# Performance work log

Measured on AMD Instinct MI355X. Metric: run time of the kernel, lower is better.

Reference implementation:

```python
import jax, jax.numpy as jnp
import numpy as np

N_NODES = 100000
N_EDGES = 3200000
IN_DIM = 64
HID = 64


def setup_inputs() -> dict:
    key = jax.random.key(0)
    ks = jax.random.split(key, 12)
    x = jax.random.normal(ks[0], (N_NODES, IN_DIM), dtype=jnp.float32)
    edge_index = jax.random.randint(ks[1], (2, N_EDGES), 0, N_NODES, dtype=jnp.int64)
    tau = jax.random.uniform(ks[2], (N_NODES, 1), dtype=jnp.float32)
    d1 = IN_DIM + 1  # augmented feature dim
    s1 = 1.0 / np.sqrt(d1)
    s2 = 1.0 / np.sqrt(HID)
    # SAGEConv: out = lin_l(mean_aggr) + lin_r(x); bias lives in lin_l. Weights stored [in, out].
    W1l = jax.random.uniform(ks[3], (d1, HID), jnp.float32, -s1, s1)
    b1l = jax.random.uniform(ks[4], (HID,), jnp.float32, -s1, s1)
    W1r = jax.random.uniform(ks[5], (d1, HID), jnp.float32, -s1, s1)
    W2l = jax.random.uniform(ks[6], (HID, HID), jnp.float32, -s2, s2)
    b2l = jax.random.uniform(ks[7], (HID,), jnp.float32, -s2, s2)
    W2r = jax.random.uniform(ks[8], (HID, HID), jnp.float32, -s2, s2)
    Wfc = jax.random.uniform(ks[9], (HID, 1), jnp.float32, -s2, s2)
    bfc = jax.random.uniform(ks[10], (1,), jnp.float32, -s2, s2)
    return {"x": x, "edge_index": edge_index, "tau": tau,
            "W1l": W1l, "b1l": b1l, "W1r": W1r,
            "W2l": W2l, "b2l": b2l, "W2r": W2r,
            "Wfc": Wfc, "bfc": bfc}


def _sage_conv(x, src, dst, Wl, bl, Wr, n_nodes):
    # mean aggregation of source-node features onto target nodes
    summed = jax.ops.segment_sum(x[src], dst, num_segments=n_nodes)  # [N, d]
    deg = jax.ops.segment_sum(jnp.ones(src.shape[0], x.dtype), dst, num_segments=n_nodes)
    mean = summed / jnp.maximum(deg, 1.0)[:, None]
    return mean @ Wl + bl + x @ Wr


def reference(x, edge_index, tau, W1l, b1l, W1r, W2l, b2l, W2r, Wfc, bfc):
    src, dst = edge_index[0], edge_index[1]
    n = x.shape[0]
    h = jnp.concatenate([x, tau], axis=1)  # augment_features: append tau column
    h = jax.nn.relu(_sage_conv(h, src, dst, W1l, b1l, W1r, n))
    h = jax.nn.relu(_sage_conv(h, src, dst, W2l, b2l, W2r, n))
    return h @ Wfc + bfc  # [N, 1]
```

## Files before the change

kernel.cpp:

```cpp
#include <hip/hip_runtime.h>
#include <hip/hip_bf16.h>
#include <hip/hip_fp16.h>


#define WAVES_PER_BLOCK 16
#define LAYER_BLOCK (WAVES_PER_BLOCK * 64)
#define LAYER_GRID 512

#define BSH 7
#define NBKT 782
#define NBLK 256

typedef _Float16 half8 __attribute__((ext_vector_type(8)));
typedef float floatx4 __attribute__((ext_vector_type(4)));


__global__ __launch_bounds__(256) void k_hist(const int* __restrict__ dst,
                                              int* __restrict__ histT, int E) {
    __shared__ int h[NBKT];
    for (int i = threadIdx.x; i < NBKT; i += 256) h[i] = 0;
    __syncthreads();
    int per = (E + NBLK - 1) / NBLK;
    int lo = blockIdx.x * per;
    int hi = lo + per; if (hi > E) hi = E;
    for (int e = lo + threadIdx.x; e < hi; e += 256)
        atomicAdd(&h[dst[e] >> BSH], 1);
    __syncthreads();
    for (int k = threadIdx.x; k < NBKT; k += 256)
        histT[k * NBLK + blockIdx.x] = h[k];
}

__global__ __launch_bounds__(NBLK) void k_scanblk(int* __restrict__ histT,
                                                  int* __restrict__ btot) {
    __shared__ int s[NBLK];
    int k = blockIdx.x, t = threadIdx.x;
    int v = histT[k * NBLK + t];
    s[t] = v;
    __syncthreads();
    for (int off = 1; off < NBLK; off <<= 1) {
        int u = (t >= off) ? s[t - off] : 0;
        __syncthreads();
        s[t] += u;
        __syncthreads();
    }
    histT[k * NBLK + t] = s[t] - v;
    if (t == NBLK - 1) btot[k] = s[t];
}

__global__ __launch_bounds__(1024) void k_scanbkt(const int* __restrict__ btot,
                                                  int* __restrict__ bstart) {
    __shared__ int s[1024];
    int t = threadIdx.x;
    int v = (t < NBKT) ? btot[t] : 0;
    s[t] = v;
    __syncthreads();
    for (int off = 1; off < 1024; off <<= 1) {
        int u = (t >= off) ? s[t - off] : 0;
        __syncthreads();
        s[t] += u;
        __syncthreads();
    }
    if (t < NBKT) bstart[t] = s[t] - v;
    if (t == NBKT - 1) bstart[NBKT] = s[t];
}

__global__ __launch_bounds__(256) void k_scatter(const int* __restrict__ src,
                                                 const int* __restrict__ dst,
                                                 const int* __restrict__ histT,
                                                 const int* __restrict__ bstart,
                                                 int* __restrict__ binned, int E) {
    __shared__ int cur[NBKT];
    int b = blockIdx.x;
    for (int k = threadIdx.x; k < NBKT; k += 256)
        cur[k] = bstart[k] + histT[k * NBLK + b];
    __syncthreads();
    int per = (E + NBLK - 1) / NBLK;
    int lo = b * per;
    int hi = lo + per; if (hi > E) hi = E;
    for (int e = lo + threadIdx.x; e < hi; e += 256) {
        int d = dst[e], s = src[e];
        int pos = atomicAdd(&cur[d >> BSH], 1);
        binned[pos] = (s << BSH) | (d & ((1 << BSH) - 1));
    }
}

__global__ __launch_bounds__(256) void k_bucket(const int* __restrict__ binned,
                                                const int* __restrict__ bstart,
                                                int* __restrict__ rowptr,
                                                int* __restrict__ deg,
                                                int* __restrict__ colidx, int N) {
    __shared__ int cnt[128], sc[128], cur[128];
    int k = blockIdx.x, t = threadIdx.x;
    int lo = bstart[k], hi = bstart[k + 1];
    if (t < 128) cnt[t] = 0;
    __syncthreads();
    for (int e = lo + t; e < hi; e += 256)
        atomicAdd(&cnt[binned[e] & 127], 1);
    __syncthreads();
    if (t < 128) sc[t] = cnt[t];
    __syncthreads();
    for (int off = 1; off < 128; off <<= 1) {
        int u = 0;
        if (t < 128 && t >= off) u = sc[t - off];
        __syncthreads();
        if (t < 128) sc[t] += u;
        __syncthreads();
    }
    if (t < 128) {
        int abs0 = lo + (sc[t] - cnt[t]);
        cur[t] = abs0;
        int gnode = (k << BSH) + t;
        if (gnode < N) { rowptr[gnode] = abs0; deg[gnode] = cnt[t]; }
    }
    __syncthreads();
    for (int e = lo + t; e < hi; e += 256) {
        int p = binned[e];
        int pos = atomicAdd(&cur[p & 127], 1);
        colidx[pos] = p >> BSH;
    }
}

__global__ __launch_bounds__(256) void k_prep(const float* __restrict__ x,
                                              __half* __restrict__ xh, int n2) {
    int i = blockIdx.x * 256 + threadIdx.x;
    if (i < n2) {
        float2 v = ((const float2*)x)[i];
        ((__half2*)xh)[i] = __floats2half2_rn(v.x, v.y);
    }
}

__global__ __launch_bounds__(256) void k_prepw(
    const float* __restrict__ W1l, const float* __restrict__ W1r,
    const float* __restrict__ W2l, const float* __restrict__ W2r,
    __half* __restrict__ wbuf1, __half* __restrict__ wbuf2) {
    int idx = blockIdx.x * 256 + threadIdx.x;
    if (idx < 1280) {
        int lane = idx & 63;
        int nt = (idx >> 6) & 3;
        int kstep = idx >> 8;
        int col = nt * 16 + (lane & 15);
        int kbase = kstep * 32 + (lane >> 4) * 8;
#pragma unroll
        for (int j = 0; j < 8; ++j) {
            int k = kbase + j;
            float v;
            if (k < 64)       v = W1l[k * 64 + col];
            else if (k < 128) v = W1r[(k - 64) * 64 + col];
            else if (k == 128) v = W1l[64 * 64 + col];
            else if (k == 129) v = W1r[64 * 64 + col];
            else v = 0.f;
            wbuf1[(size_t)idx * 8 + j] = __float2half(v);
        }
    } else if (idx < 1280 + 1024) {
        int i2 = idx - 1280;
        int lane = i2 & 63;
        int nt = (i2 >> 6) & 3;
        int kstep = i2 >> 8;
        int col = nt * 16 + (lane & 15);
        int kbase = kstep * 32 + (lane >> 4) * 8;
#pragma unroll
        for (int j = 0; j < 8; ++j) {
            int k = kbase + j;
            float v = (k < 64) ? W2l[k * 64 + col] : W2r[(k - 64) * 64 + col];
            wbuf2[(size_t)i2 * 8 + j] = __float2half(v);
        }
    }
}


__device__ __forceinline__ int pair_idx(int sidx, int j2, int half) {
    return __builtin_amdgcn_ds_bpermute(((j2 + half) << 2), sidx);
}

__global__ __launch_bounds__(LAYER_BLOCK) void k_aggr1(
    const __half* __restrict__ xh, const float* __restrict__ tau,
    const int* __restrict__ rowptr, const int* __restrict__ deg,
    const int* __restrict__ colidx,
    __half* __restrict__ zm1, __half* __restrict__ mt1, int N) {
    int lane = threadIdx.x & 63;
    int half = lane >> 5;
    int c2 = (lane & 31) << 1;
    int wave = blockIdx.x * WAVES_PER_BLOCK + (threadIdx.x >> 6);
    int nwaves = gridDim.x * WAVES_PER_BLOCK;

    for (int node = wave; node < N; node += nwaves) {
        int start = rowptr[node];
        int d = deg[node];
        float2 A0 = {0.f, 0.f}, A1 = {0.f, 0.f}, A2 = {0.f, 0.f}, A3 = {0.f, 0.f};
        float sumtau = 0.f;
        for (int base = 0; base < d; base += 64) {
            int n = d - base;
            if (n > 64) n = 64;
            int sidx = 0;
            if (lane < n) {
                sidx = colidx[start + base + lane];
                sumtau += tau[sidx];
            }
            int npair = n >> 1;
            int j = 0;
            for (; j + 4 <= npair; j += 4) {
                int i0 = pair_idx(sidx, (j + 0) << 1, half);
                int i1 = pair_idx(sidx, (j + 1) << 1, half);
                int i2 = pair_idx(sidx, (j + 2) << 1, half);
                int i3 = pair_idx(sidx, (j + 3) << 1, half);
                float2 v0 = __half22float2(*(const __half2*)(xh + ((size_t)(unsigned)i0 << 6) + c2));
                float2 v1 = __half22float2(*(const __half2*)(xh + ((size_t)(unsigned)i1 << 6) + c2));
                float2 v2 = __half22float2(*(const __half2*)(xh + ((size_t)(unsigned)i2 << 6) + c2));
                float2 v3 = __half22float2(*(const __half2*)(xh + ((size_t)(unsigned)i3 << 6) + c2));
                A0.x += v0.x; A0.y += v0.y;
                A1.x += v1.x; A1.y += v1.y;
                A2.x += v2.x; A2.y += v2.y;
                A3.x += v3.x; A3.y += v3.y;
            }
            for (; j < npair; ++j) {
                int i0 = pair_idx(sidx, j << 1, half);
                float2 v0 = __half22float2(*(const __half2*)(xh + ((size_t)(unsigned)i0 << 6) + c2));
                A0.x += v0.x; A0.y += v0.y;
            }
            if (n & 1) {
                int il = __builtin_amdgcn_ds_bpermute((n - 1) << 2, sidx);
                if (lane < 32) {
                    float2 v = __half22float2(*(const __half2*)(xh + ((size_t)(unsigned)il << 6) + c2));
                    A0.x += v.x; A0.y += v.y;
                }
            }
        }
        float2 A;
        A.x = (A0.x + A1.x) + (A2.x + A3.x);
        A.y = (A0.y + A1.y) + (A2.y + A3.y);
        A.x += __shfl_xor(A.x, 32, 64);
        A.y += __shfl_xor(A.y, 32, 64);
#pragma unroll
        for (int off = 32; off > 0; off >>= 1) sumtau += __shfl_down(sumtau, off, 64);

        float inv = 1.f / fmaxf((float)d, 1.f);
        if (lane < 32)
            ((__half2*)(zm1 + (size_t)node * 64))[lane] =
                __floats2half2_rn(A.x * inv, A.y * inv);
        if (lane == 0) mt1[node] = __float2half(sumtau * inv);
    }
}

__global__ __launch_bounds__(LAYER_BLOCK) void k_aggr2(
    const __half* __restrict__ h1,
    const int* __restrict__ rowptr, const int* __restrict__ deg,
    const int* __restrict__ colidx, __half* __restrict__ zm2, int N) {
    int lane = threadIdx.x & 63;
    int half = lane >> 5;
    int c2 = (lane & 31) << 1;
    int wave = blockIdx.x * WAVES_PER_BLOCK + (threadIdx.x >> 6);
    int nwaves = gridDim.x * WAVES_PER_BLOCK;

    for (int node = wave; node < N; node += nwaves) {
        int start = rowptr[node];
        int d = deg[node];
        float2 A0 = {0.f, 0.f}, A1 = {0.f, 0.f}, A2 = {0.f, 0.f}, A3 = {0.f, 0.f};
        for (int base = 0; base < d; base += 64) {
            int n = d - base;
            if (n > 64) n = 64;
            int sidx = 0;
            if (lane < n) sidx = colidx[start + base + lane];
            int npair = n >> 1;
            int j = 0;
            for (; j + 4 <= npair; j += 4) {
                int i0 = pair_idx(sidx, (j + 0) << 1, half);
                int i1 = pair_idx(sidx, (j + 1) << 1, half);
                int i2 = pair_idx(sidx, (j + 2) << 1, half);
                int i3 = pair_idx(sidx, (j + 3) << 1, half);
                float2 v0 = __half22float2(*(const __half2*)(h1 + ((size_t)(unsigned)i0 << 6) + c2));
                float2 v1 = __half22float2(*(const __half2*)(h1 + ((size_t)(unsigned)i1 << 6) + c2));
                float2 v2 = __half22float2(*(const __half2*)(h1 + ((size_t)(unsigned)i2 << 6) + c2));
                float2 v3 = __half22float2(*(const __half2*)(h1 + ((size_t)(unsigned)i3 << 6) + c2));
                A0.x += v0.x; A0.y += v0.y;
                A1.x += v1.x; A1.y += v1.y;
                A2.x += v2.x; A2.y += v2.y;
                A3.x += v3.x; A3.y += v3.y;
            }
            for (; j < npair; ++j) {
                int i0 = pair_idx(sidx, j << 1, half);
                float2 v0 = __half22float2(*(const __half2*)(h1 + ((size_t)(unsigned)i0 << 6) + c2));
                A0.x += v0.x; A0.y += v0.y;
            }
            if (n & 1) {
                int il = __builtin_amdgcn_ds_bpermute((n - 1) << 2, sidx);
                if (lane < 32) {
                    float2 v = __half22float2(*(const __half2*)(h1 + ((size_t)(unsigned)il << 6) + c2));
                    A0.x += v.x; A0.y += v.y;
                }
            }
        }
        float2 A;
        A.x = (A0.x + A1.x) + (A2.x + A3.x);
        A.y = (A0.y + A1.y) + (A2.y + A3.y);
        A.x += __shfl_xor(A.x, 32, 64);
        A.y += __shfl_xor(A.y, 32, 64);
        float inv = 1.f / fmaxf((float)d, 1.f);
        if (lane < 32)
            ((__half2*)(zm2 + (size_t)node * 64))[lane] =
                __floats2half2_rn(A.x * inv, A.y * inv);
    }
}


__global__ __launch_bounds__(256) void k_gemm1(
    const __half* __restrict__ zm1, const __half* __restrict__ mt1,
    const __half* __restrict__ xh, const float* __restrict__ tau,
    const __half* __restrict__ wbuf1, const float* __restrict__ b1l,
    __half* __restrict__ h1, int ntiles) {
    int tile = blockIdx.x * 4 + (threadIdx.x >> 6);
    if (tile >= ntiles) return;
    int lane = threadIdx.x & 63;
    int sub = lane & 15;
    int quad = lane >> 4;
    int row = tile * 16 + sub;

    floatx4 acc0 = {0.f, 0.f, 0.f, 0.f};
    floatx4 acc1 = {0.f, 0.f, 0.f, 0.f};
    floatx4 acc2 = {0.f, 0.f, 0.f, 0.f};
    floatx4 acc3 = {0.f, 0.f, 0.f, 0.f};

    const _Float16* zrow = (const _Float16*)zm1 + (size_t)row * 64 + quad * 8;
    const _Float16* xrow = (const _Float16*)xh + (size_t)row * 64 + quad * 8;
    const _Float16* wb = (const _Float16*)wbuf1 + (size_t)lane * 8;

    half8 amat[5];
    amat[0] = *(const half8*)(zrow);
    amat[1] = *(const half8*)(zrow + 32);
    amat[2] = *(const half8*)(xrow);
    amat[3] = *(const half8*)(xrow + 32);
    half8 a4 = {0, 0, 0, 0, 0, 0, 0, 0};
    if (quad == 0) {
        a4[0] = ((const _Float16*)mt1)[row];
        a4[1] = (_Float16)tau[row];
    }
    amat[4] = a4;

#pragma unroll
    for (int ks = 0; ks < 5; ++ks) {
        half8 a = amat[ks];
        half8 b0 = *(const half8*)(wb + (size_t)(ks * 4 + 0) * 512);
        half8 b1 = *(const half8*)(wb + (size_t)(ks * 4 + 1) * 512);
        half8 b2 = *(const half8*)(wb + (size_t)(ks * 4 + 2) * 512);
        half8 b3 = *(const half8*)(wb + (size_t)(ks * 4 + 3) * 512);
        acc0 = __builtin_amdgcn_mfma_f32_16x16x32_f16(a, b0, acc0, 0, 0, 0);
        acc1 = __builtin_amdgcn_mfma_f32_16x16x32_f16(a, b1, acc1, 0, 0, 0);
        acc2 = __builtin_amdgcn_mfma_f32_16x16x32_f16(a, b2, acc2, 0, 0, 0);
        acc3 = __builtin_amdgcn_mfma_f32_16x16x32_f16(a, b3, acc3, 0, 0, 0);
    }
    float bv0 = b1l[sub], bv1 = b1l[16 + sub], bv2 = b1l[32 + sub], bv3 = b1l[48 + sub];
#pragma unroll
    for (int reg = 0; reg < 4; ++reg) {
        int r = quad * 4 + reg;
        __half* orow = h1 + (size_t)(tile * 16 + r) * 64;
        orow[sub]      = __float2half(fmaxf(acc0[reg] + bv0, 0.f));
        orow[16 + sub] = __float2half(fmaxf(acc1[reg] + bv1, 0.f));
        orow[32 + sub] = __float2half(fmaxf(acc2[reg] + bv2, 0.f));
        orow[48 + sub] = __float2half(fmaxf(acc3[reg] + bv3, 0.f));
    }
}

__global__ __launch_bounds__(256) void k_gemm2(
    const __half* __restrict__ zm2, const __half* __restrict__ h1,
    const __half* __restrict__ wbuf2, const float* __restrict__ b2l,
    const float* __restrict__ Wfc, const float* __restrict__ bfc,
    float* __restrict__ out, int ntiles) {
    int tile = blockIdx.x * 4 + (threadIdx.x >> 6);
    if (tile >= ntiles) return;
    int lane = threadIdx.x & 63;
    int sub = lane & 15;
    int quad = lane >> 4;
    int row = tile * 16 + sub;

    floatx4 acc0 = {0.f, 0.f, 0.f, 0.f};
    floatx4 acc1 = {0.f, 0.f, 0.f, 0.f};
    floatx4 acc2 = {0.f, 0.f, 0.f, 0.f};
    floatx4 acc3 = {0.f, 0.f, 0.f, 0.f};

    const _Float16* zrow = (const _Float16*)zm2 + (size_t)row * 64 + quad * 8;
    const _Float16* hrow = (const _Float16*)h1 + (size_t)row * 64 + quad * 8;
    const _Float16* wb = (const _Float16*)wbuf2 + (size_t)lane * 8;

    half8 amat[4];
    amat[0] = *(const half8*)(zrow);
    amat[1] = *(const half8*)(zrow + 32);
    amat[2] = *(const half8*)(hrow);
    amat[3] = *(const half8*)(hrow + 32);

#pragma unroll
    for (int ks = 0; ks < 4; ++ks) {
        half8 a = amat[ks];
        half8 b0 = *(const half8*)(wb + (size_t)(ks * 4 + 0) * 512);
        half8 b1 = *(const half8*)(wb + (size_t)(ks * 4 + 1) * 512);
        half8 b2 = *(const half8*)(wb + (size_t)(ks * 4 + 2) * 512);
        half8 b3 = *(const half8*)(wb + (size_t)(ks * 4 + 3) * 512);
        acc0 = __builtin_amdgcn_mfma_f32_16x16x32_f16(a, b0, acc0, 0, 0, 0);
        acc1 = __builtin_amdgcn_mfma_f32_16x16x32_f16(a, b1, acc1, 0, 0, 0);
        acc2 = __builtin_amdgcn_mfma_f32_16x16x32_f16(a, b2, acc2, 0, 0, 0);
        acc3 = __builtin_amdgcn_mfma_f32_16x16x32_f16(a, b3, acc3, 0, 0, 0);
    }
    float bb0 = b2l[sub], bb1 = b2l[16 + sub], bb2 = b2l[32 + sub], bb3 = b2l[48 + sub];
    float wv0 = Wfc[sub], wv1 = Wfc[16 + sub], wv2 = Wfc[32 + sub], wv3 = Wfc[48 + sub];
    float p[4];
#pragma unroll
    for (int reg = 0; reg < 4; ++reg) {
        p[reg] = fmaxf(acc0[reg] + bb0, 0.f) * wv0
               + fmaxf(acc1[reg] + bb1, 0.f) * wv1
               + fmaxf(acc2[reg] + bb2, 0.f) * wv2
               + fmaxf(acc3[reg] + bb3, 0.f) * wv3;
    }
#pragma unroll
    for (int m = 1; m <= 8; m <<= 1) {
#pragma unroll
        for (int reg = 0; reg < 4; ++reg) p[reg] += __shfl_xor(p[reg], m, 64);
    }
    if (sub == 0) {
        float b0 = bfc[0];
#pragma unroll
        for (int reg = 0; reg < 4; ++reg)
            out[tile * 16 + quad * 4 + reg] = p[reg] + b0;
    }
}

extern "C" void kernel_launch(void* const* d_in, const int* in_sizes, int n_in,
                              void* d_out, int out_size, void* d_ws, size_t ws_size,
                              hipStream_t stream) {
    const float* x   = (const float*)d_in[0];
    const int*   ei  = (const int*)d_in[1];
    const float* tau = (const float*)d_in[2];
    const float* W1l = (const float*)d_in[3];
    const float* b1l = (const float*)d_in[4];
    const float* W1r = (const float*)d_in[5];
    const float* W2l = (const float*)d_in[6];
    const float* b2l = (const float*)d_in[7];
    const float* W2r = (const float*)d_in[8];
    const float* Wfc = (const float*)d_in[9];
    const float* bfc = (const float*)d_in[10];
    float* out = (float*)d_out;

    const int N = in_sizes[0] / 64;
    const int E = in_sizes[1] / 2;
    const int* src = ei;
    const int* dst = ei + E;

    char* w = (char*)d_ws;
    auto take = [&](size_t b) { char* p = w; w += (b + 255) & ~(size_t)255; return p; };
    int*    histT  = (int*)take((size_t)NBKT * NBLK * 4);
    int*    btot   = (int*)take((size_t)NBKT * 4);
    int*    bstart = (int*)take((size_t)(NBKT + 1) * 4);
    int*    binned = (int*)take((size_t)E * 4);
    int*    rowptr = (int*)take((size_t)N * 4);
    int*    deg    = (int*)take((size_t)N * 4);
    int*    colidx = (int*)take((size_t)E * 4);
    __half* xh     = (__half*)take((size_t)N * 64 * 2);
    __half* h1     = (__half*)take((size_t)N * 64 * 2);
    __half* zm1    = (__half*)take((size_t)N * 64 * 2);
    __half* mt1    = (__half*)take((size_t)N * 2);
    __half* zm2    = (__half*)take((size_t)N * 64 * 2);
    __half* wbuf1  = (__half*)take(1280 * 8 * 2);
    __half* wbuf2  = (__half*)take(1024 * 8 * 2);

    int n2 = N * 32;
    int ntiles = N / 16;
    int gblocks = (ntiles + 3) / 4;

    k_hist   <<<NBLK, 256, 0, stream>>>(dst, histT, E);
    k_scanblk<<<NBKT, NBLK, 0, stream>>>(histT, btot);
    k_scanbkt<<<1, 1024, 0, stream>>>(btot, bstart);
    k_scatter<<<NBLK, 256, 0, stream>>>(src, dst, histT, bstart, binned, E);
    k_bucket <<<NBKT, 256, 0, stream>>>(binned, bstart, rowptr, deg, colidx, N);
    k_prep   <<<(n2 + 255) / 256, 256, 0, stream>>>(x, xh, n2);
    k_prepw  <<<9, 256, 0, stream>>>(W1l, W1r, W2l, W2r, wbuf1, wbuf2);
    k_aggr1  <<<LAYER_GRID, LAYER_BLOCK, 0, stream>>>(xh, tau, rowptr, deg, colidx, zm1, mt1, N);
    k_gemm1  <<<gblocks, 256, 0, stream>>>(zm1, mt1, xh, tau, wbuf1, b1l, h1, ntiles);
    k_aggr2  <<<LAYER_GRID, LAYER_BLOCK, 0, stream>>>(h1, rowptr, deg, colidx, zm2, N);
    k_gemm2  <<<gblocks, 256, 0, stream>>>(zm2, h1, wbuf2, b2l, Wfc, bfc, out, ntiles);
}
```

Baseline: 308.9 us.

## Process two nodes per wave in aggregation kernels and merge prep kernels

The aggregation kernels now give each half-wave its own destination node instead of splitting one node's edges across both halves. This drops the cross-half reduction, and each wave covers two rows per iteration. The two halves can have different degrees, so shorter rows sit masked while the longer one finishes, which may waste lanes. The x-to-half conversion and weight packing are merged into one launch to save a kernel launch. N must be even, or the last node is skipped.

```diff
diff --git a/kernel.cpp b/kernel.cpp
--- a/kernel.cpp
+++ b/kernel.cpp
@@ -120,57 +120,53 @@
     }
 }
 
-__global__ __launch_bounds__(256) void k_prep(const float* __restrict__ x,
-                                              __half* __restrict__ xh, int n2) {
-    int i = blockIdx.x * 256 + threadIdx.x;
-    if (i < n2) {
-        float2 v = ((const float2*)x)[i];
-        ((__half2*)xh)[i] = __floats2half2_rn(v.x, v.y);
-    }
-}
-
-__global__ __launch_bounds__(256) void k_prepw(
+__global__ __launch_bounds__(256) void k_prepall(
+    const float* __restrict__ x, __half* __restrict__ xh, int n2,
     const float* __restrict__ W1l, const float* __restrict__ W1r,
     const float* __restrict__ W2l, const float* __restrict__ W2r,
     __half* __restrict__ wbuf1, __half* __restrict__ wbuf2) {
-    int idx = blockIdx.x * 256 + threadIdx.x;
-    if (idx < 1280) {
-        int lane = idx & 63;
-        int nt = (idx >> 6) & 3;
-        int kstep = idx >> 8;
-        int col = nt * 16 + (lane & 15);
-        int kbase = kstep * 32 + (lane >> 4) * 8;
-#pragma unroll
-        for (int j = 0; j < 8; ++j) {
-            int k = kbase + j;
-            float v;
-            if (k < 64)       v = W1l[k * 64 + col];
-            else if (k < 128) v = W1r[(k - 64) * 64 + col];
-            else if (k == 128) v = W1l[64 * 64 + col];
-            else if (k == 129) v = W1r[64 * 64 + col];
-            else v = 0.f;
-            wbuf1[(size_t)idx * 8 + j] = __float2half(v);
+    if (blockIdx.x < 9) {
+        int idx = blockIdx.x * 256 + threadIdx.x;
+        if (idx < 1280) {
+            int lane = idx & 63;
+            int nt = (idx >> 6) & 3;
+            int kstep = idx >> 8;
+            int col = nt * 16 + (lane & 15);
+            int kbase = kstep * 32 + (lane >> 4) * 8;
+#pragma unroll
+            for (int j = 0; j < 8; ++j) {
+                int k = kbase + j;
+                float v;
+                if (k < 64)        v = W1l[k * 64 + col];
+                else if (k < 128)  v = W1r[(k - 64) * 64 + col];
+                else if (k == 128) v = W1l[64 * 64 + col];
+                else if (k == 129) v = W1r[64 * 64 + col];
+                else v = 0.f;
+                wbuf1[(size_t)idx * 8 + j] = __float2half(v);
+            }
+        } else if (idx < 1280 + 1024) {
+            int i2 = idx - 1280;
+            int lane = i2 & 63;
+            int nt = (i2 >> 6) & 3;
+            int kstep = i2 >> 8;
+            int col = nt * 16 + (lane & 15);
+            int kbase = kstep * 32 + (lane >> 4) * 8;
+#pragma unroll
+            for (int j = 0; j < 8; ++j) {
+                int k = kbase + j;
+                float v = (k < 64) ? W2l[k * 64 + col] : W2r[(k - 64) * 64 + col];
+                wbuf2[(size_t)i2 * 8 + j] = __float2half(v);
+            }
         }
-    } else if (idx < 1280 + 1024) {
-        int i2 = idx - 1280;
-        int lane = i2 & 63;
-        int nt = (i2 >> 6) & 3;
-        int kstep = i2 >> 8;
-        int col = nt * 16 + (lane & 15);
-        int kbase = kstep * 32 + (lane >> 4) * 8;
-#pragma unroll
-        for (int j = 0; j < 8; ++j) {
-            int k = kbase + j;
-            float v = (k < 64) ? W2l[k * 64 + col] : W2r[(k - 64) * 64 + col];
-            wbuf2[(size_t)i2 * 8 + j] = __float2half(v);
+    } else {
+        int i = (blockIdx.x - 9) * 256 + threadIdx.x;
+        if (i < n2) {
+            float2 v = ((const float2*)x)[i];
+            ((__half2*)xh)[i] = __floats2half2_rn(v.x, v.y);
         }
     }
 }
 
-
-__device__ __forceinline__ int pair_idx(int sidx, int j2, int half) {
-    return __builtin_amdgcn_ds_bpermute(((j2 + half) << 2), sidx);
-}
 
 __global__ __launch_bounds__(LAYER_BLOCK) void k_aggr1(
     const __half* __restrict__ xh, const float* __restrict__ tau,
@@ -179,65 +175,56 @@
     __half* __restrict__ zm1, __half* __restrict__ mt1, int N) {
     int lane = threadIdx.x & 63;
     int half = lane >> 5;
-    int c2 = (lane & 31) << 1;
+    int c = lane & 31;
     int wave = blockIdx.x * WAVES_PER_BLOCK + (threadIdx.x >> 6);
     int nwaves = gridDim.x * WAVES_PER_BLOCK;
-
-    for (int node = wave; node < N; node += nwaves) {
+    int npairs = N >> 1;
+
+    for (int pair = wave; pair < npairs; pair += nwaves) {
+        int node = pair * 2 + half;
         int start = rowptr[node];
         int d = deg[node];
         float2 A0 = {0.f, 0.f}, A1 = {0.f, 0.f}, A2 = {0.f, 0.f}, A3 = {0.f, 0.f};
         float sumtau = 0.f;
-        for (int base = 0; base < d; base += 64) {
+        for (int base = 0; base < d || base < __shfl_xor(d, 32, 64); base += 32) {
             int n = d - base;
-            if (n > 64) n = 64;
+            n = (n < 0) ? 0 : (n > 32 ? 32 : n);
+            int nmax = max(n, __shfl_xor(n, 32, 64));
             int sidx = 0;
-            if (lane < n) {
-                sidx = colidx[start + base + lane];
+            if (c < n) {
+                sidx = colidx[start + base + c];
                 sumtau += tau[sidx];
             }
-            int npair = n >> 1;
             int j = 0;
-            for (; j + 4 <= npair; j += 4) {
-                int i0 = pair_idx(sidx, (j + 0) << 1, half);
-                int i1 = pair_idx(sidx, (j + 1) << 1, half);
-                int i2 = pair_idx(sidx, (j + 2) << 1, half);
-                int i3 = pair_idx(sidx, (j + 3) << 1, half);
-                float2 v0 = __half22float2(*(const __half2*)(xh + ((size_t)(unsigned)i0 << 6) + c2));
-                float2 v1 = __half22float2(*(const __half2*)(xh + ((size_t)(unsigned)i1 << 6) + c2));
-                float2 v2 = __half22float2(*(const __half2*)(xh + ((size_t)(unsigned)i2 << 6) + c2));
-                float2 v3 = __half22float2(*(const __half2*)(xh + ((size_t)(unsigned)i3 << 6) + c2));
-                A0.x += v0.x; A0.y += v0.y;
-                A1.x += v1.x; A1.y += v1.y;
-                A2.x += v2.x; A2.y += v2.y;
-                A3.x += v3.x; A3.y += v3.y;
-            }
-            for (; j < npair; ++j) {
-                int i0 = pair_idx(sidx, j << 1, half);
-                float2 v0 = __half22float2(*(const __half2*)(xh + ((size_t)(unsigned)i0 << 6) + c2));
-                A0.x += v0.x; A0.y += v0.y;
-            }
-            if (n & 1) {
-                int il = __builtin_amdgcn_ds_bpermute((n - 1) << 2, sidx);
-                if (lane < 32) {
-                    float2 v = __half22float2(*(const __half2*)(xh + ((size_t)(unsigned)il << 6) + c2));
-                    A0.x += v.x; A0.y += v.y;
-                }
+            for (; j + 4 <= nmax; j += 4) {
+                int i0 = __builtin_amdgcn_ds_bpermute((half * 32 + j + 0) << 2, sidx);
+                int i1 = __builtin_amdgcn_ds_bpermute((half * 32 + j + 1) << 2, sidx);
+                int i2 = __builtin_amdgcn_ds_bpermute((half * 32 + j + 2) << 2, sidx);
+                int i3 = __builtin_amdgcn_ds_bpermute((half * 32 + j + 3) << 2, sidx);
+                float2 v0 = __half22float2(*(const __half2*)(xh + ((size_t)(unsigned)i0 << 6) + (c << 1)));
+                float2 v1 = __half22float2(*(const __half2*)(xh + ((size_t)(unsigned)i1 << 6) + (c << 1)));
+                float2 v2 = __half22float2(*(const __half2*)(xh + ((size_t)(unsigned)i2 << 6) + (c << 1)));
+                float2 v3 = __half22float2(*(const __half2*)(xh + ((size_t)(unsigned)i3 << 6) + (c << 1)));
+                if (j + 0 < n) { A0.x += v0.x; A0.y += v0.y; }
+                if (j + 1 < n) { A1.x += v1.x; A1.y += v1.y; }
+                if (j + 2 < n) { A2.x += v2.x; A2.y += v2.y; }
+                if (j + 3 < n) { A3.x += v3.x; A3.y += v3.y; }
+            }
+            for (; j < nmax; ++j) {
+                int i0 = __builtin_amdgcn_ds_bpermute((half * 32 + j) << 2, sidx);
+                float2 v0 = __half22float2(*(const __half2*)(xh + ((size_t)(unsigned)i0 << 6) + (c << 1)));
+                if (j < n) { A0.x += v0.x; A0.y += v0.y; }
             }
         }
         float2 A;
         A.x = (A0.x + A1.x) + (A2.x + A3.x);
         A.y = (A0.y + A1.y) + (A2.y + A3.y);
-        A.x += __shfl_xor(A.x, 32, 64);
-        A.y += __shfl_xor(A.y, 32, 64);
-#pragma unroll
-        for (int off = 32; off > 0; off >>= 1) sumtau += __shfl_down(sumtau, off, 64);
+#pragma unroll
+        for (int off = 16; off > 0; off >>= 1) sumtau += __shfl_xor(sumtau, off, 64);
 
         float inv = 1.f / fmaxf((float)d, 1.f);
-        if (lane < 32)
-            ((__half2*)(zm1 + (size_t)node * 64))[lane] =
-                __floats2half2_rn(A.x * inv, A.y * inv);
-        if (lane == 0) mt1[node] = __float2half(sumtau * inv);
+        ((__half2*)(zm1 + (size_t)node * 64))[c] = __floats2half2_rn(A.x * inv, A.y * inv);
+        if (c == 0) mt1[node] = __float2half(sumtau * inv);
     }
 }
 
@@ -247,57 +234,48 @@
     const int* __restrict__ colidx, __half* __restrict__ zm2, int N) {
     int lane = threadIdx.x & 63;
     int half = lane >> 5;
-    int c2 = (lane & 31) << 1;
+    int c = lane & 31;
     int wave = blockIdx.x * WAVES_PER_BLOCK + (threadIdx.x >> 6);
     int nwaves = gridDim.x * WAVES_PER_BLOCK;
-
-    for (int node = wave; node < N; node += nwaves) {
+    int npairs = N >> 1;
+
+    for (int pair = wave; pair < npairs; pair += nwaves) {
+        int node = pair * 2 + half;
         int start = rowptr[node];
         int d = deg[node];
         float2 A0 = {0.f, 0.f}, A1 = {0.f, 0.f}, A2 = {0.f, 0.f}, A3 = {0.f, 0.f};
-        for (int base = 0; base < d; base += 64) {
+        for (int base = 0; base < d || base < __shfl_xor(d, 32, 64); base += 32) {
             int n = d - base;
-            if (n > 64) n = 64;
+            n = (n < 0) ? 0 : (n > 32 ? 32 : n);
+            int nmax = max(n, __shfl_xor(n, 32, 64));
             int sidx = 0;
-            if (lane < n) sidx = colidx[start + base + lane];
-            int npair = n >> 1;
+            if (c < n) sidx = colidx[start + base + c];
             int j = 0;
-            for (; j + 4 <= npair; j += 4) {
-                int i0 = pair_idx(sidx, (j + 0) << 1, half);
-                int i1 = pair_idx(sidx, (j + 1) << 1, half);
-                int i2 = pair_idx(sidx, (j + 2) << 1, half);
-                int i3 = pair_idx(sidx, (j + 3) << 1, half);
-                float2 v0 = __half22float2(*(const __half2*)(h1 + ((size_t)(unsigned)i0 << 6) + c2));
-                float2 v1 = __half22float2(*(const __half2*)(h1 + ((size_t)(unsigned)i1 << 6) + c2));
-                float2 v2 = __half22float2(*(const __half2*)(h1 + ((size_t)(unsigned)i2 << 6) + c2));
-                float2 v3 = __half22float2(*(const __half2*)(h1 + ((size_t)(unsigned)i3 << 6) + c2));
-                A0.x += v0.x; A0.y += v0.y;
-                A1.x += v1.x; A1.y += v1.y;
-                A2.x += v2.x; A2.y += v2.y;
-                A3.x += v3.x; A3.y += v3.y;
-            }
-            for (; j < npair; ++j) {
-                int i0 = pair_idx(sidx, j << 1, half);
-                float2 v0 = __half22float2(*(const __half2*)(h1 + ((size_t)(unsigned)i0 << 6) + c2));
-                A0.x += v0.x; A0.y += v0.y;
-            }
-            if (n & 1) {
-                int il = __builtin_amdgcn_ds_bpermute((n - 1) << 2, sidx);
-                if (lane < 32) {
-                    float2 v = __half22float2(*(const __half2*)(h1 + ((size_t)(unsigned)il << 6) + c2));
-                    A0.x += v.x; A0.y += v.y;
-                }
+            for (; j + 4 <= nmax; j += 4) {
+                int i0 = __builtin_amdgcn_ds_bpermute((half * 32 + j + 0) << 2, sidx);
+                int i1 = __builtin_amdgcn_ds_bpermute((half * 32 + j + 1) << 2, sidx);
+                int i2 = __builtin_amdgcn_ds_bpermute((half * 32 + j + 2) << 2, sidx);
+                int i3 = __builtin_amdgcn_ds_bpermute((half * 32 + j + 3) << 2, sidx);
+                float2 v0 = __half22float2(*(const __half2*)(h1 + ((size_t)(unsigned)i0 << 6) + (c << 1)));
+                float2 v1 = __half22float2(*(const __half2*)(h1 + ((size_t)(unsigned)i1 << 6) + (c << 1)));
+                float2 v2 = __half22float2(*(const __half2*)(h1 + ((size_t)(unsigned)i2 << 6) + (c << 1)));
+                float2 v3 = __half22float2(*(const __half2*)(h1 + ((size_t)(unsigned)i3 << 6) + (c << 1)));
+                if (j + 0 < n) { A0.x += v0.x; A0.y += v0.y; }
+                if (j + 1 < n) { A1.x += v1.x; A1.y += v1.y; }
+                if (j + 2 < n) { A2.x += v2.x; A2.y += v2.y; }
+                if (j + 3 < n) { A3.x += v3.x; A3.y += v3.y; }
+            }
+            for (; j < nmax; ++j) {
+                int i0 = __builtin_amdgcn_ds_bpermute((half * 32 + j) << 2, sidx);
+                float2 v0 = __half22float2(*(const __half2*)(h1 + ((size_t)(unsigned)i0 << 6) + (c << 1)));
+                if (j < n) { A0.x += v0.x; A0.y += v0.y; }
             }
         }
         float2 A;
         A.x = (A0.x + A1.x) + (A2.x + A3.x);
         A.y = (A0.y + A1.y) + (A2.y + A3.y);
-        A.x += __shfl_xor(A.x, 32, 64);
-        A.y += __shfl_xor(A.y, 32, 64);
         float inv = 1.f / fmaxf((float)d, 1.f);
-        if (lane < 32)
-            ((__half2*)(zm2 + (size_t)node * 64))[lane] =
-                __floats2half2_rn(A.x * inv, A.y * inv);
+        ((__half2*)(zm2 + (size_t)node * 64))[c] = __floats2half2_rn(A.x * inv, A.y * inv);
     }
 }
 
@@ -460,6 +438,7 @@
     __half* wbuf2  = (__half*)take(1024 * 8 * 2);
 
     int n2 = N * 32;
+    int pblocks = 9 + (n2 + 255) / 256;
     int ntiles = N / 16;
     int gblocks = (ntiles + 3) / 4;
 
@@ -468,8 +447,7 @@
     k_scanbkt<<<1, 1024, 0, stream>>>(btot, bstart);
     k_scatter<<<NBLK, 256, 0, stream>>>(src, dst, histT, bstart, binned, E);
     k_bucket <<<NBKT, 256, 0, stream>>>(binned, bstart, rowptr, deg, colidx, N);
-    k_prep   <<<(n2 + 255) / 256, 256, 0, stream>>>(x, xh, n2);
-    k_prepw  <<<9, 256, 0, stream>>>(W1l, W1r, W2l, W2r, wbuf1, wbuf2);
+    k_prepall<<<pblocks, 256, 0, stream>>>(x, xh, n2, W1l, W1r, W2l, W2r, wbuf1, wbuf2);
     k_aggr1  <<<LAYER_GRID, LAYER_BLOCK, 0, stream>>>(xh, tau, rowptr, deg, colidx, zm1, mt1, N);
     k_gemm1  <<<gblocks, 256, 0, stream>>>(zm1, mt1, xh, tau, wbuf1, b1l, h1, ntiles);
     k_aggr2  <<<LAYER_GRID, LAYER_BLOCK, 0, stream>>>(h1, rowptr, deg, colidx, zm2, N);
```

Measured after the change: 305.8 us. Within noise of the previous version (-1.0%).
